# Kernel tuning notes

Hardware: AMD Instinct MI355X
Metric: run time of the kernel (lower is better)

The kernel has to match this reference:

```python
import jax, jax.numpy as jnp
import numpy as np

EMBED_DIM = 1024
NUM_HEADS = 16
HEAD_DIM = EMBED_DIM // NUM_HEADS
SCALE = HEAD_DIM ** -0.5


def setup_inputs() -> dict:
    key = jax.random.key(0)
    ks = jax.random.split(key, 5)
    B, N, D = 2, 2048, EMBED_DIM
    std = D ** -0.5
    x = jax.random.normal(ks[0], (B, N, D), dtype=jnp.float32)
    W_qkv = jax.random.normal(ks[1], (D, 3 * D), dtype=jnp.float32) * std
    b_qkv = jnp.zeros((3 * D,), dtype=jnp.float32)
    W_proj = jax.random.normal(ks[2], (D, D), dtype=jnp.float32) * std
    b_proj = jnp.zeros((D,), dtype=jnp.float32)
    return {"x": x, "W_qkv": W_qkv, "b_qkv": b_qkv, "W_proj": W_proj, "b_proj": b_proj}


def reference(x, W_qkv, b_qkv, W_proj, b_proj):
    B, N, D = x.shape
    H, Hd = NUM_HEADS, HEAD_DIM
    qkv = x @ W_qkv + b_qkv                      # (B, N, 3D)
    qkv = qkv.reshape(B, N, 3, H, Hd)
    q = qkv[:, :, 0].transpose(0, 2, 1, 3)       # (B, H, N, Hd)
    k = qkv[:, :, 1].transpose(0, 2, 1, 3)
    v = qkv[:, :, 2].transpose(0, 2, 1, 3)
    attn = jnp.einsum('bhqd,bhkd->bhqk', q, k) * SCALE  # (B, H, N, N)
    attn = jax.nn.softmax(attn, axis=-1)
    out = jnp.einsum('bhqk,bhkd->bhqd', attn, v)        # (B, H, N, Hd)
    out = out.transpose(0, 2, 1, 3).reshape(B, N, D)
    return out @ W_proj + b_proj
```

## Files before the change

kernel.cpp:

```cpp
#include <hip/hip_runtime.h>
#include <stdint.h>

#define BATCH 2
#define NH 16
#define SEQ 2048
#define DIM 1024
#define HD 64
#define MROWS (BATCH*SEQ)

typedef __attribute__((ext_vector_type(8))) _Float16 f16x8;
typedef __attribute__((ext_vector_type(16))) float f32x16;
typedef __attribute__((ext_vector_type(4))) float f32x4;
typedef __attribute__((ext_vector_type(2))) __fp16 fp16x2;
typedef __attribute__((ext_vector_type(4))) short short4v;
typedef __attribute__((ext_vector_type(2))) unsigned uint2v;

__device__ __forceinline__ short f2h(float f) {
  union { _Float16 h; short s; } u;
  u.h = (_Float16)f;
  return u.s;
}

__device__ __forceinline__ float fast_exp2(float x) {
#if __has_builtin(__builtin_amdgcn_exp2f)
  return __builtin_amdgcn_exp2f(x);
#else
  return exp2f(x);
#endif
}

__device__ __forceinline__ unsigned pk2(float a, float b) {
  union { fp16x2 h; unsigned u; } x;
  x.h = __builtin_amdgcn_cvt_pkrtz(a, b);
  return x.u;
}

__device__ __forceinline__ void perm32swap(unsigned &a, unsigned &b) {
#if __has_builtin(__builtin_amdgcn_permlane32_swap)
  uint2v r = __builtin_amdgcn_permlane32_swap(a, b, false, false);
  a = r[0]; b = r[1];
#else
  unsigned as = (unsigned)__shfl_xor((int)a, 32);
  unsigned bs = (unsigned)__shfl_xor((int)b, 32);
  bool lo = ((threadIdx.x & 63) < 32);
  unsigned na = lo ? a : bs;
  unsigned nb = lo ? as : b;
  a = na; b = nb;
#endif
}

__device__ __forceinline__ void async_load16(const void* g, void* l) {
  __builtin_amdgcn_global_load_lds((const __attribute__((address_space(1))) void*)g,
                                   (__attribute__((address_space(3))) void*)l, 16, 0, 0);
}

__global__ __launch_bounds__(256) void k_cvt(const float* __restrict__ in,
                                             short* __restrict__ out, int n4) {
  int i = blockIdx.x * 256 + threadIdx.x;
  if (i >= n4) return;
  float4 v = ((const float4*)in)[i];
  short4v o;
  o[0] = f2h(v.x); o[1] = f2h(v.y); o[2] = f2h(v.z); o[3] = f2h(v.w);
  ((short4v*)out)[i] = o;
}

__global__ __launch_bounds__(256) void k_transpose(const float* __restrict__ in,
                                                   short* __restrict__ out,
                                                   int K, int N) {
  __shared__ float t[32][33];
  int n0 = blockIdx.x * 32, k0 = blockIdx.y * 32;
  int tx = threadIdx.x, ty = threadIdx.y;
  #pragma unroll
  for (int i = 0; i < 32; i += 8)
    t[ty + i][tx] = in[(size_t)(k0 + ty + i) * N + (n0 + tx)];
  __syncthreads();
  #pragma unroll
  for (int i = 0; i < 32; i += 8)
    out[(size_t)(n0 + ty + i) * K + (k0 + tx)] = f2h(t[tx][ty + i]);
}

template <int MODE, int BM>
__global__ __launch_bounds__(256) void k_gemm_bt(
    const short* __restrict__ A, const short* __restrict__ Bt,
    const float* __restrict__ bias,
    short* __restrict__ Qd, short* __restrict__ Kd, short* __restrict__ Vtd,
    float* __restrict__ Cf, int Ncols, int Kdim) {
  constexpr int BN = 128, BK = 64;
  constexpr int RI = BM / 32;
  __shared__ short Al[2][BM * BK];
  __shared__ short Bl[2][BN * BK];
  const int tid = threadIdx.x;
  const int lane = tid & 63;
  const int wid = tid >> 6;
  const int wr = wid >> 1, wc = wid & 1;
  const int m0 = blockIdx.y * BM, n0 = blockIdx.x * BN;
  const int l15 = lane & 15, lk = (lane >> 4) * 8;

  f32x4 acc[RI][4] = {};

  auto stage = [&](int kt, int buf) {
    int k0 = kt * BK;
    #pragma unroll
    for (int i2 = 0; i2 < BM / 32; i2++) {
      int c = i2 * 256 + tid;
      int r = c >> 3, cs = (c & 7) * 8;
      async_load16(A + (size_t)(m0 + r) * Kdim + k0 + (cs ^ ((r & 7) * 8)),
                   &Al[buf][c * 8]);
    }
    #pragma unroll
    for (int i2 = 0; i2 < 4; i2++) {
      int c = i2 * 256 + tid;
      int r = c >> 3, cs = (c & 7) * 8;
      async_load16(Bt + (size_t)(n0 + r) * Kdim + k0 + (cs ^ ((r & 7) * 8)),
                   &Bl[buf][c * 8]);
    }
  };

  auto compute = [&](int buf) {
    f16x8 af[2][RI], bfr[2][4];
    #pragma unroll
    for (int kk = 0; kk < 2; kk++) {
      #pragma unroll
      for (int i = 0; i < RI; i++) {
        int row = wr * (BM / 2) + i * 16 + l15;
        af[kk][i] = *(const f16x8*)&Al[buf][row * 64 + ((kk * 32 + lk) ^ ((row & 7) * 8))];
      }
      #pragma unroll
      for (int j = 0; j < 4; j++) {
        int row = wc * 64 + j * 16 + l15;
        bfr[kk][j] = *(const f16x8*)&Bl[buf][row * 64 + ((kk * 32 + lk) ^ ((row & 7) * 8))];
      }
    }
    __builtin_amdgcn_s_setprio(1);
    #pragma unroll
    for (int i = 0; i < RI; i++)
      #pragma unroll
      for (int j = 0; j < 4; j++) {
        acc[i][j] = __builtin_amdgcn_mfma_f32_16x16x32_f16(af[0][i], bfr[0][j], acc[i][j], 0, 0, 0);
        acc[i][j] = __builtin_amdgcn_mfma_f32_16x16x32_f16(af[1][i], bfr[1][j], acc[i][j], 0, 0, 0);
      }
    __builtin_amdgcn_s_setprio(0);
  };

  stage(0, 0);
  const int NT = Kdim / BK;
  for (int t = 0; t < NT; t++) {
    int cur = t & 1;
    if (t + 1 < NT) {
      stage(t + 1, cur ^ 1);
      if constexpr (BM == 128) asm volatile("s_waitcnt vmcnt(8)" ::: "memory");
      else                     asm volatile("s_waitcnt vmcnt(6)" ::: "memory");
    } else {
      asm volatile("s_waitcnt vmcnt(0)" ::: "memory");
    }
    __builtin_amdgcn_s_barrier();
    __builtin_amdgcn_sched_barrier(0);
    compute(cur);
    __builtin_amdgcn_sched_barrier(0);
    __builtin_amdgcn_s_barrier();
  }

  const int rl = (lane >> 4) * 4;
  if (MODE == 0) {
    #pragma unroll
    for (int j = 0; j < 4; j++) {
      int col = n0 + wc * 64 + j * 16 + l15;
      float bv = bias[col];
      int sec = col >> 10;
      int cc = col & 1023;
      int h = cc >> 6, hd = cc & 63;
      float mul = (sec == 0) ? (0.125f * 1.44269504088896f) : 1.0f;
      #pragma unroll
      for (int i = 0; i < RI; i++) {
        int rowb = m0 + wr * (BM / 2) + i * 16 + rl;
        #pragma unroll
        for (int r = 0; r < 4; r++) {
          int row = rowb + r;
          int b = row >> 11, nr = row & 2047;
          short v = f2h((acc[i][j][r] + bv) * mul);
          size_t bh = (size_t)(b * NH + h);
          size_t base2 = bh * (size_t)(SEQ * HD);
          if (sec == 0) {
            Qd[base2 + (size_t)nr * HD + hd] = v;
          } else if (sec == 1) {
            Kd[base2 + (size_t)(((nr >> 5) * 4 + (hd >> 4)) * 512 +
                                (((hd >> 3) & 1) * 32 + (nr & 31)) * 8 + (hd & 7))] = v;
          } else {
            Vtd[base2 + (size_t)(((nr >> 4) * 2 + (hd >> 5)) * 512 +
                                 (((nr >> 3) & 1) * 32 + (hd & 31)) * 8 + (nr & 7))] = v;
          }
        }
      }
    }
  } else {
    #pragma unroll
    for (int j = 0; j < 4; j++) {
      int col = n0 + wc * 64 + j * 16 + l15;
      float bv = bias[col];
      #pragma unroll
      for (int i = 0; i < RI; i++) {
        int rowb = m0 + wr * (BM / 2) + i * 16 + rl;
        #pragma unroll
        for (int r = 0; r < 4; r++)
          Cf[(size_t)(rowb + r) * Ncols + col] = acc[i][j][r] + bv;
      }
    }
  }
}

#define QBLK 64
#define NKVT (SEQ / 64)

#define PACK8(sv, R0, lsv, OUT) do {                                        \
    float e0_ = fast_exp2((sv)[R0 + 0]), e1_ = fast_exp2((sv)[R0 + 1]);     \
    float e2_ = fast_exp2((sv)[R0 + 2]), e3_ = fast_exp2((sv)[R0 + 3]);     \
    float e4_ = fast_exp2((sv)[R0 + 4]), e5_ = fast_exp2((sv)[R0 + 5]);     \
    float e6_ = fast_exp2((sv)[R0 + 6]), e7_ = fast_exp2((sv)[R0 + 7]);     \
    lsv += ((e0_ + e1_) + (e2_ + e3_)) + ((e4_ + e5_) + (e6_ + e7_));       \
    unsigned u0_ = pk2(e0_, e1_), u1_ = pk2(e2_, e3_);                      \
    unsigned u2_ = pk2(e4_, e5_), u3_ = pk2(e6_, e7_);                      \
    perm32swap(u0_, u2_);                                                   \
    perm32swap(u1_, u3_);                                                   \
    union { unsigned u[4]; f16x8 v; } W_;                                   \
    W_.u[0] = u0_; W_.u[1] = u1_; W_.u[2] = u2_; W_.u[3] = u3_;             \
    OUT = W_.v;                                                             \
  } while (0)

__global__ __launch_bounds__(256) void k_flash(const short* __restrict__ Qd,
                                               const short* __restrict__ KB,
                                               const short* __restrict__ VB,
                                               short* __restrict__ Od) {
  __shared__ short Kl[2][4096];
  __shared__ short Vl[2][4096];
  const int tid = threadIdx.x;
  const int lane = tid & 63;
  const int w = tid >> 6;
  const int wq = w >> 1;
  const int kvh = w & 1;
  const int l31 = lane & 31, lh = lane >> 5;
  const int bh = blockIdx.x;
  const int q0 = blockIdx.y * QBLK + wq * 32;
  const size_t base = (size_t)bh * (size_t)(SEQ * HD);

  f16x8 qf[4];
  #pragma unroll
  for (int ds = 0; ds < 4; ds++)
    qf[ds] = *(const f16x8*)(Qd + base + (size_t)(q0 + l31) * HD + ds * 16 + lh * 8);

  f32x16 o[2] = {};
  float lsum = 0.f;

#define STAGE(kvt, buf) do {                                                \
    const short* ks_ = KB + base + (size_t)(kvt) * 4096;                    \
    const short* vs_ = VB + base + (size_t)(kvt) * 4096;                    \
    async_load16(ks_ + tid * 8, &Kl[buf][tid * 8]);                         \
    async_load16(ks_ + (tid + 256) * 8, &Kl[buf][(tid + 256) * 8]);         \
    async_load16(vs_ + tid * 8, &Vl[buf][tid * 8]);                         \
    async_load16(vs_ + (tid + 256) * 8, &Vl[buf][(tid + 256) * 8]);         \
  } while (0)

  auto compute = [&](int cur) {
    f16x8 kf[4];
    #pragma unroll
    for (int ds = 0; ds < 4; ds++)
      kf[ds] = *(const f16x8*)&Kl[cur][((kvh * 4 + ds) * 64 + lane) * 8];
    f32x16 s = {};
    __builtin_amdgcn_s_setprio(1);
    #pragma unroll
    for (int ds = 0; ds < 4; ds++)
      s = __builtin_amdgcn_mfma_f32_32x32x16_f16(kf[ds], qf[ds], s, 0, 0, 0);
    __builtin_amdgcn_s_setprio(0);
    f16x8 vf[2][2];
    #pragma unroll
    for (int ks = 0; ks < 2; ks++)
      #pragma unroll
      for (int hdt = 0; hdt < 2; hdt++)
        vf[ks][hdt] = *(const f16x8*)&Vl[cur][(((kvh * 2 + ks) * 2 + hdt) * 64 + lane) * 8];
    f16x8 p[2];
    PACK8(s, 0, lsum, p[0]); PACK8(s, 8, lsum, p[1]);
    __builtin_amdgcn_s_setprio(1);
    #pragma unroll
    for (int ks = 0; ks < 2; ks++) {
      o[0] = __builtin_amdgcn_mfma_f32_32x32x16_f16(p[ks], vf[ks][0], o[0], 0, 0, 0);
      o[1] = __builtin_amdgcn_mfma_f32_32x32x16_f16(p[ks], vf[ks][1], o[1], 0, 0, 0);
    }
    __builtin_amdgcn_s_setprio(0);
  };

  STAGE(0, 0);
  for (int kvt = 0; kvt < NKVT; kvt++) {
    int cur = kvt & 1;
    if (kvt + 1 < NKVT) {
      STAGE(kvt + 1, cur ^ 1);
      asm volatile("s_waitcnt vmcnt(4)" ::: "memory");
    } else {
      asm volatile("s_waitcnt vmcnt(0)" ::: "memory");
    }
    __builtin_amdgcn_s_barrier();
    __builtin_amdgcn_sched_barrier(0);
    compute(cur);
    __builtin_amdgcn_sched_barrier(0);
    __builtin_amdgcn_s_barrier();
  }
#undef STAGE

  float* ob = (float*)&Kl[0][0];
  float* lb = (float*)&Vl[0][0];
  if (kvh == 1) {
    #pragma unroll
    for (int hdt = 0; hdt < 2; hdt++)
      #pragma unroll
      for (int rq = 0; rq < 4; rq++) {
        f32x4 v4;
        v4[0] = o[hdt][rq * 4 + 0]; v4[1] = o[hdt][rq * 4 + 1];
        v4[2] = o[hdt][rq * 4 + 2]; v4[3] = o[hdt][rq * 4 + 3];
        *(f32x4*)&ob[wq * 2048 + (hdt * 4 + rq) * 256 + lane * 4] = v4;
      }
    lb[wq * 64 + lane] = lsum;
  }
  __syncthreads();
  if (kvh == 0) {
    #pragma unroll
    for (int hdt = 0; hdt < 2; hdt++)
      #pragma unroll
      for (int rq = 0; rq < 4; rq++) {
        f32x4 v4 = *(const f32x4*)&ob[wq * 2048 + (hdt * 4 + rq) * 256 + lane * 4];
        o[hdt][rq * 4 + 0] += v4[0]; o[hdt][rq * 4 + 1] += v4[1];
        o[hdt][rq * 4 + 2] += v4[2]; o[hdt][rq * 4 + 3] += v4[3];
      }
    lsum += lb[wq * 64 + lane];

    lsum += __shfl_xor(lsum, 32);
    float inv = 1.f / lsum;
    const int b = bh >> 4, h = bh & 15;
    #pragma unroll
    for (int reg = 0; reg < 16; reg++) {
      int qrow = (reg & 3) + 8 * (reg >> 2) + 4 * lh;
      float s = __shfl(inv, qrow);
      size_t r0 = (size_t)(b * SEQ + q0 + qrow) * DIM + h * 64;
      Od[r0 + l31]      = f2h(o[0][reg] * s);
      Od[r0 + 32 + l31] = f2h(o[1][reg] * s);
    }
  }
}

extern "C" void kernel_launch(void* const* d_in, const int* in_sizes, int n_in,
                              void* d_out, int out_size, void* d_ws, size_t ws_size,
                              hipStream_t stream) {
  const float* x     = (const float*)d_in[0];
  const float* Wqkv  = (const float*)d_in[1];
  const float* bqkv  = (const float*)d_in[2];
  const float* Wproj = (const float*)d_in[3];
  const float* bproj = (const float*)d_in[4];
  float* out = (float*)d_out;

  char* ws = (char*)d_ws;
  short* x_h    = (short*)(ws);
  short* Wqkv_t = (short*)(ws + ((size_t)8  << 20));
  short* Wproj_t= (short*)(ws + ((size_t)14 << 20));
  short* Qd     = (short*)(ws + ((size_t)16 << 20));
  short* Kd     = (short*)(ws + ((size_t)24 << 20));
  short* Vtd    = (short*)(ws + ((size_t)32 << 20));
  short* Od     = (short*)(ws + ((size_t)40 << 20));

  k_cvt<<<(MROWS * DIM / 4 + 255) / 256, 256, 0, stream>>>(x, x_h, MROWS * DIM / 4);
  dim3 tb(32, 8);
  k_transpose<<<dim3(3 * DIM / 32, DIM / 32), tb, 0, stream>>>(Wqkv, Wqkv_t, DIM, 3 * DIM);
  k_transpose<<<dim3(DIM / 32, DIM / 32), tb, 0, stream>>>(Wproj, Wproj_t, DIM, DIM);
  k_gemm_bt<0, 128><<<dim3(3 * DIM / 128, MROWS / 128), 256, 0, stream>>>(
      x_h, Wqkv_t, bqkv, Qd, Kd, Vtd, nullptr, 3 * DIM, DIM);
  k_flash<<<dim3(BATCH * NH, SEQ / QBLK), 256, 0, stream>>>(Qd, Kd, Vtd, Od);
  k_gemm_bt<1, 64><<<dim3(DIM / 128, MROWS / 64), 256, 0, stream>>>(
      Od, Wproj_t, bproj, nullptr, nullptr, nullptr, out, DIM, DIM);
}
```

Measured before the change: 139.4 us.

## Load K/V fragments directly from global into registers, dropping LDS staging

The flash-attention kernel no longer stages K and V tiles through double-buffered shared memory with async loads and barriers. Each wave now loads its own K/V fragments straight from global memory into registers, with a two-deep register ping-pong that prefetches the next tile. This removes the LDS round trip and the per-iteration block barriers. In exchange it adds register pressure and relies on L2/cache for K/V reuse across the two query waves that read the same half. Shared memory is kept only for the final cross-wave reduction.

```diff
diff --git a/kernel.cpp b/kernel.cpp
--- a/kernel.cpp
+++ b/kernel.cpp
@@ -230,8 +230,8 @@
                                                const short* __restrict__ KB,
                                                const short* __restrict__ VB,
                                                short* __restrict__ Od) {
-  __shared__ short Kl[2][4096];
-  __shared__ short Vl[2][4096];
+  __shared__ float ob[4096];
+  __shared__ float lb[128];
   const int tid = threadIdx.x;
   const int lane = tid & 63;
   const int w = tid >> 6;
@@ -247,65 +247,56 @@
   for (int ds = 0; ds < 4; ds++)
     qf[ds] = *(const f16x8*)(Qd + base + (size_t)(q0 + l31) * HD + ds * 16 + lh * 8);
 
+  const short* kb = KB + base + kvh * 2048 + (size_t)lane * 8;
+  const short* vb = VB + base + kvh * 2048 + (size_t)lane * 8;
+
   f32x16 o[2] = {};
   float lsum = 0.f;
 
-#define STAGE(kvt, buf) do {                                                \
-    const short* ks_ = KB + base + (size_t)(kvt) * 4096;                    \
-    const short* vs_ = VB + base + (size_t)(kvt) * 4096;                    \
-    async_load16(ks_ + tid * 8, &Kl[buf][tid * 8]);                         \
-    async_load16(ks_ + (tid + 256) * 8, &Kl[buf][(tid + 256) * 8]);         \
-    async_load16(vs_ + tid * 8, &Vl[buf][tid * 8]);                         \
-    async_load16(vs_ + (tid + 256) * 8, &Vl[buf][(tid + 256) * 8]);         \
+#define LOADK(t, kf) do {                                                   \
+    const short* p_ = kb + (size_t)(t) * 4096;                              \
+    kf[0] = *(const f16x8*)(p_);                                            \
+    kf[1] = *(const f16x8*)(p_ + 512);                                      \
+    kf[2] = *(const f16x8*)(p_ + 1024);                                     \
+    kf[3] = *(const f16x8*)(p_ + 1536);                                     \
   } while (0)
-
-  auto compute = [&](int cur) {
-    f16x8 kf[4];
-    #pragma unroll
-    for (int ds = 0; ds < 4; ds++)
-      kf[ds] = *(const f16x8*)&Kl[cur][((kvh * 4 + ds) * 64 + lane) * 8];
+#define LOADV(t, vf) do {                                                   \
+    const short* p_ = vb + (size_t)(t) * 4096;                              \
+    vf[0] = *(const f16x8*)(p_);                               \
+    vf[1] = *(const f16x8*)(p_ + 512);                         \
+    vf[2] = *(const f16x8*)(p_ + 1024);                        \
+    vf[3] = *(const f16x8*)(p_ + 1536);                        \
+  } while (0)
+
+  auto compute = [&](const f16x8* kf, const f16x8* vf) {
     f32x16 s = {};
     __builtin_amdgcn_s_setprio(1);
     #pragma unroll
     for (int ds = 0; ds < 4; ds++)
       s = __builtin_amdgcn_mfma_f32_32x32x16_f16(kf[ds], qf[ds], s, 0, 0, 0);
     __builtin_amdgcn_s_setprio(0);
-    f16x8 vf[2][2];
-    #pragma unroll
-    for (int ks = 0; ks < 2; ks++)
-      #pragma unroll
-      for (int hdt = 0; hdt < 2; hdt++)
-        vf[ks][hdt] = *(const f16x8*)&Vl[cur][(((kvh * 2 + ks) * 2 + hdt) * 64 + lane) * 8];
     f16x8 p[2];
     PACK8(s, 0, lsum, p[0]); PACK8(s, 8, lsum, p[1]);
     __builtin_amdgcn_s_setprio(1);
     #pragma unroll
     for (int ks = 0; ks < 2; ks++) {
-      o[0] = __builtin_amdgcn_mfma_f32_32x32x16_f16(p[ks], vf[ks][0], o[0], 0, 0, 0);
-      o[1] = __builtin_amdgcn_mfma_f32_32x32x16_f16(p[ks], vf[ks][1], o[1], 0, 0, 0);
+      o[0] = __builtin_amdgcn_mfma_f32_32x32x16_f16(p[ks], vf[ks * 2 + 0], o[0], 0, 0, 0);
+      o[1] = __builtin_amdgcn_mfma_f32_32x32x16_f16(p[ks], vf[ks * 2 + 1], o[1], 0, 0, 0);
     }
     __builtin_amdgcn_s_setprio(0);
   };
 
-  STAGE(0, 0);
-  for (int kvt = 0; kvt < NKVT; kvt++) {
-    int cur = kvt & 1;
-    if (kvt + 1 < NKVT) {
-      STAGE(kvt + 1, cur ^ 1);
-      asm volatile("s_waitcnt vmcnt(4)" ::: "memory");
-    } else {
-      asm volatile("s_waitcnt vmcnt(0)" ::: "memory");
-    }
-    __builtin_amdgcn_s_barrier();
-    __builtin_amdgcn_sched_barrier(0);
-    compute(cur);
-    __builtin_amdgcn_sched_barrier(0);
-    __builtin_amdgcn_s_barrier();
-  }
-#undef STAGE
-
-  float* ob = (float*)&Kl[0][0];
-  float* lb = (float*)&Vl[0][0];
+  f16x8 kA[4], vA[4], kB_[4], vB_[4];
+  LOADK(0, kA); LOADV(0, vA);
+  for (int t = 0; t < NKVT; t += 2) {
+    if (t + 1 < NKVT) { LOADK(t + 1, kB_); LOADV(t + 1, vB_); }
+    compute(kA, vA);
+    if (t + 2 < NKVT) { LOADK(t + 2, kA); LOADV(t + 2, vA); }
+    if (t + 1 < NKVT) compute(kB_, vB_);
+  }
+#undef LOADK
+#undef LOADV
+
   if (kvh == 1) {
     #pragma unroll
     for (int hdt = 0; hdt < 2; hdt++)
```

After: 131.1 us. 1.06x faster.
